# Performance work log

Measured on AMD Instinct MI355X. Metric: run time of the kernel, lower is better.

## Reference

```python
import jax, jax.numpy as jnp
import numpy as np

V, D, L, S = 32000, 512, 4096, 256
LOG2 = float(np.log(2.0))


def _self_conflict(a, span):
    # a: [S, l] bool. Sequential: a[i] = a[i] & ~a[i-1] (using updated values).
    def step1(prev, cur):
        out = cur & ~prev
        return out, out
    first = a[:, 0]
    _, rest = jax.lax.scan(step1, first, a[:, 1:].T)  # scan over token axis
    a = jnp.concatenate([first[:, None], rest.T], axis=1)
    if span == 3:
        # second pass: a[i] = a[i] & ~a[i-2] on the updated array
        def step2(carry, cur):
            pm2, pm1 = carry
            out = cur & ~pm2
            return (pm1, out), out
        _, rest2 = jax.lax.scan(step2, (a[:, 0], a[:, 1]), a[:, 2:].T)
        a = jnp.concatenate([a[:, :2], rest2.T], axis=1)
    return a


def _shift_into(a1, off, L2):
    # hit[j] |= a1[j - off], zeros elsewhere
    B, l1 = a1.shape
    out = jnp.zeros((B, L2), dtype=bool)
    if off >= 0:
        end = min(L2, off + l1)
        return out.at[:, off:end].set(a1[:, :end - off])
    return out.at[:, :l1 + off].set(a1[:, -off:])


def _intersec_conflict(a1, a2, flag=False):
    # a2[j] cleared if any overlapping a1 span is active (set of shifts)
    l1, l2 = a1.shape[1], a2.shape[1]
    hit = jnp.zeros_like(a2)
    for i in range(l2 - l1 + 1):
        hit = hit | _shift_into(a1, i, l2)
    if flag:
        hit = hit | _shift_into(a1, -1, l2) | _shift_into(a1, 2, l2)
    return a2 & ~hit


def _forward(x, embd, w1, b1, w2, b2, w3, b3, g1, g2, g3, align1, align2, align3):
    emb = embd[x]                                   # [1, L, D]
    s2 = (emb[:, 1:] + emb[:, :-1]) / 2             # [1, L-1, D]
    s3 = (emb[:, 2:] + emb[:, 1:-1] + emb[:, :-2]) / 3
    heads = ((emb, w1, b1, g1, align1), (s2, w2, b2, g2, align2), (s3, w3, b3, g3, align3))
    stats, bools = [], []
    for spans, w, b, g, amask in heads:
        logits = spans @ w + b                      # [1, l, 2]
        logp = jax.nn.log_softmax(logits, axis=-1)
        p = jnp.exp(logp)
        nent = -(p * logp).sum(-1) / LOG2           # normalized entropy (2 classes)
        idx = jnp.argmax(logp + g, axis=-1)         # [S, l] Gumbel-max categorical sample
        act = jax.nn.one_hot(idx, 2, dtype=logp.dtype)
        bools.append((idx == 0) & amask[None, :])   # reduce chosen AND aligned
        stats.append((logp, nent, act))

    b1_, b2_, b3_ = bools
    b3_ = _self_conflict(b3_, 3)
    b2_ = _intersec_conflict(b3_, b2_, flag=True)
    b1_ = _intersec_conflict(b3_, b1_)
    b2_ = _self_conflict(b2_, 2)
    b1_ = _intersec_conflict(b2_, b1_)

    logp1, ne1, act1 = stats[0]
    logp2, ne2, _ = stats[1]
    logp3, ne3, _ = stats[2]
    # actions 2/3 are rewritten from the conflict-reduced booleans; action 1 keeps its sample
    act2 = jnp.stack([b2_, ~b2_], axis=-1).astype(logp2.dtype)
    act3 = jnp.stack([b3_, ~b3_], axis=-1).astype(logp3.dtype)

    nll1 = -(act1 * logp1).sum(-1).sum(1)           # [S]
    nll2 = -(act2 * logp2).sum(-1).sum(1)
    nll3 = -(act3 * logp3).sum(-1).sum(1)
    nsamp = act1.shape[0]
    nent = jnp.broadcast_to((ne1.mean(1) + ne2.mean(1) + ne3.mean(1)) / 3.0, (nsamp,))
    return nent, nll1 + nll2 + nll3, b1_, b2_, b3_


def setup_inputs():
    key = jax.random.key(0)
    k = jax.random.split(key, 11)
    x = jax.random.randint(k[0], (1, L), 0, V)
    embd = jax.random.normal(k[1], (V, D), jnp.float32) * 0.02
    w1 = jax.random.normal(k[2], (D, 2), jnp.float32) * 0.05
    w2 = jax.random.normal(k[3], (D, 2), jnp.float32) * 0.05
    w3 = jax.random.normal(k[4], (D, 2), jnp.float32) * 0.05
    b1 = jnp.zeros((2,), jnp.float32)
    b2 = jnp.zeros((2,), jnp.float32)
    b3 = jnp.zeros((2,), jnp.float32)
    g1 = jax.random.gumbel(k[5], (S, L, 2), jnp.float32)
    g2 = jax.random.gumbel(k[6], (S, L - 1, 2), jnp.float32)
    g3 = jax.random.gumbel(k[7], (S, L - 2, 2), jnp.float32)
    align1 = jax.random.randint(k[8], (L,), 0, 2).astype(bool)
    align2 = jax.random.randint(k[9], (L - 1,), 0, 2).astype(bool)
    align3 = jax.random.randint(k[10], (L - 2,), 0, 2).astype(bool)
    return {"x": x, "sample_num": S, "align1": align1, "align2": align2, "align3": align3,
            "embd": embd, "w1": w1, "b1": b1, "w2": w2, "b2": b2, "w3": w3, "b3": b3,
            "g1": g1, "g2": g2, "g3": g3}


def reference(x, sample_num, align1, align2, align3, embd, w1, b1, w2, b2, w3, b3, g1, g2, g3):
    return _forward(x, embd, w1, b1, w2, b2, w3, b3, g1, g2, g3, align1, align2, align3)
```

## Files before the change

### kernel.cpp

```cpp
#include <hip/hip_runtime.h>
#include <stdint.h>

#define L_ 4096
#define S_ 256
#define D_ 512
#define NW 64

static __device__ const float LN2F = 0.69314718055994530942f;

__global__ __launch_bounds__(256)
void k_rows(const int* __restrict__ x, const float* __restrict__ embd,
            const float* __restrict__ w1, const float* __restrict__ b1,
            const float* __restrict__ w2, const float* __restrict__ b2,
            const float* __restrict__ w3, const float* __restrict__ b3,
            float* __restrict__ lp, float* __restrict__ entbuf) {
    const int wid  = threadIdx.x >> 6;
    const int lane = threadIdx.x & 63;
    const int t = blockIdx.x * 4 + wid;
    const int t1 = (t + 1 < L_) ? t + 1 : t;
    const int t2 = (t + 2 < L_) ? t + 2 : t;
    const int d0 = lane * 8;

    const float4* e0p = (const float4*)(embd + (size_t)x[t]  * D_ + d0);
    const float4* e1p = (const float4*)(embd + (size_t)x[t1] * D_ + d0);
    const float4* e2p = (const float4*)(embd + (size_t)x[t2] * D_ + d0);
    float4 e0a = e0p[0], e0b = e0p[1];
    float4 e1a = e1p[0], e1b = e1p[1];
    float4 e2a = e2p[0], e2b = e2p[1];
    const float4* w1p = (const float4*)(w1 + 2 * d0);
    const float4* w2p = (const float4*)(w2 + 2 * d0);
    const float4* w3p = (const float4*)(w3 + 2 * d0);

    float v0[8] = {e0a.x,e0a.y,e0a.z,e0a.w,e0b.x,e0b.y,e0b.z,e0b.w};
    float v1[8] = {e1a.x,e1a.y,e1a.z,e1a.w,e1b.x,e1b.y,e1b.z,e1b.w};
    float v2[8] = {e2a.x,e2a.y,e2a.z,e2a.w,e2b.x,e2b.y,e2b.z,e2b.w};
    float wv1[16], wv2[16], wv3[16];
    for (int q = 0; q < 4; q++) {
        float4 a = w1p[q]; wv1[4*q]=a.x; wv1[4*q+1]=a.y; wv1[4*q+2]=a.z; wv1[4*q+3]=a.w;
        float4 b = w2p[q]; wv2[4*q]=b.x; wv2[4*q+1]=b.y; wv2[4*q+2]=b.z; wv2[4*q+3]=b.w;
        float4 c = w3p[q]; wv3[4*q]=c.x; wv3[4*q+1]=c.y; wv3[4*q+2]=c.z; wv3[4*q+3]=c.w;
    }
    double a0=0,a1=0,a2=0,a3=0,a4=0,a5=0;
    #pragma unroll
    for (int j = 0; j < 8; j++) {
        float s2 = (v1[j] + v0[j]) * 0.5f;
        float s3 = ((v2[j] + v1[j]) + v0[j]) / 3.0f;
        a0 += (double)v0[j] * (double)wv1[2*j];
        a1 += (double)v0[j] * (double)wv1[2*j+1];
        a2 += (double)s2    * (double)wv2[2*j];
        a3 += (double)s2    * (double)wv2[2*j+1];
        a4 += (double)s3    * (double)wv3[2*j];
        a5 += (double)s3    * (double)wv3[2*j+1];
    }
    #pragma unroll
    for (int o = 32; o > 0; o >>= 1) {
        a0 += __shfl_xor(a0, o, 64);
        a1 += __shfl_xor(a1, o, 64);
        a2 += __shfl_xor(a2, o, 64);
        a3 += __shfl_xor(a3, o, 64);
        a4 += __shfl_xor(a4, o, 64);
        a5 += __shfl_xor(a5, o, 64);
    }
    if (lane < 3) {
        double l0, l1; const float* bb;
        if (lane == 0)      { l0 = a0; l1 = a1; bb = b1; }
        else if (lane == 1) { l0 = a2; l1 = a3; bb = b2; }
        else                { l0 = a4; l1 = a5; bb = b3; }
        bool valid = (lane == 0) || (lane == 1 && t < L_-1) || (lane == 2 && t < L_-2);
        float ev = 0.0f;
        if (valid) {
            l0 += (double)bb[0]; l1 += (double)bb[1];
            double m = fmax(l0, l1);
            double sa = l0 - m, sb = l1 - m;
            double lse = log(exp(sa) + exp(sb));
            float p0l = (float)(sa - lse), p1l = (float)(sb - lse);
            lp[2*lane*L_ + t] = p0l; lp[(2*lane+1)*L_ + t] = p1l;
            float p0 = expf(p0l), p1 = expf(p1l);
            ev = -(p0*p0l + p1*p1l) / LN2F;
        }
        entbuf[lane*L_ + t] = ev;
    }
}

__device__ __forceinline__ uint64_t pass1_noc(uint64_t wp) {
    uint64_t o = wp & ~(wp << 1);
    uint64_t h = wp & (wp << 1);
    o |= (o << 2)  & h; h &= (h << 2);
    o |= (o << 4)  & h; h &= (h << 4);
    o |= (o << 8)  & h; h &= (h << 8);
    o |= (o << 16) & h; h &= (h << 16);
    o |= (o << 32) & h;
    return o;
}
__device__ __forceinline__ uint64_t pass2_noc(uint64_t ap) {
    uint64_t o = ap & ~(ap << 2);
    uint64_t h = ap & (ap << 2);
    o |= (o << 4)  & h; h &= (h << 4);
    o |= (o << 8)  & h; h &= (h << 8);
    o |= (o << 16) & h; h &= (h << 16);
    o |= (o << 32) & h;
    return o;
}

__global__ __launch_bounds__(1024)
void k_fused(const float* __restrict__ lp,
             const int* __restrict__ al1, const int* __restrict__ al2, const int* __restrict__ al3,
             const float2* __restrict__ g1, const float2* __restrict__ g2, const float2* __restrict__ g3,
             const float* __restrict__ entbuf, float* __restrict__ out) {
    const int s = blockIdx.x;
    const int tid = threadIdx.x;
    const int lane = tid & 63;
    const int wv = tid >> 6;

    __shared__ uint64_t w1s[NW], w2s[NW], w3s[NW];
    __shared__ uint64_t o1s[NW], o2s[NW], o3s[NW];

    float lp2a[4], lp2b[4], lp3a[4], lp3b[4];
    float nllacc = 0.0f;
    #pragma unroll
    for (int it = 0; it < 4; it++) {
        const int t = it * 1024 + tid;
        float2 v1 = g1[(size_t)s * L_ + t];
        float lp0 = lp[t], lp1v = lp[L_ + t];
        bool raw1 = (lp0 + v1.x) >= (lp1v + v1.y);
        bool m1 = raw1 && (al1[t] != 0);
        nllacc += raw1 ? -lp0 : -lp1v;
        bool m2 = false, m3 = false;
        lp2a[it] = 0.f; lp2b[it] = 0.f; lp3a[it] = 0.f; lp3b[it] = 0.f;
        if (t < L_-1) {
            float2 v2 = g2[(size_t)s * (L_-1) + t];
            float a = lp[2*L_+t], b = lp[3*L_+t];
            lp2a[it] = a; lp2b[it] = b;
            m2 = ((a + v2.x) >= (b + v2.y)) && (al2[t] != 0);
        }
        if (t < L_-2) {
            float2 v3 = g3[(size_t)s * (L_-2) + t];
            float a = lp[4*L_+t], b = lp[5*L_+t];
            lp3a[it] = a; lp3b[it] = b;
            m3 = ((a + v3.x) >= (b + v3.y)) && (al3[t] != 0);
        }
        unsigned long long b1b = __ballot(m1);
        unsigned long long b2b = __ballot(m2);
        unsigned long long b3b = __ballot(m3);
        if (lane == 0) {
            int w = t >> 6;
            w1s[w] = b1b; w2s[w] = b2b; w3s[w] = b3b;
        }
    }
    __syncthreads();

    if (wv == 0) {
        const int j = lane;
        uint64_t w3 = w3s[j];
        uint64_t oA = pass1_noc(w3);
        uint64_t oB = pass1_noc(w3 & ~1ull);
        unsigned F = (unsigned)(oA >> 63) | (((unsigned)(oB >> 63)) << 1);
        #pragma unroll
        for (int d = 1; d < 64; d <<= 1) {
            unsigned P = __shfl_up(F, d, 64);
            if (lane >= d) {
                unsigned la = P & 1, lb = (P >> 1) & 1;
                unsigned ra = F & 1, rb = (F >> 1) & 1;
                F = (la ? rb : ra) | ((lb ? rb : ra) << 1);
            }
        }
        unsigned Fp = __shfl_up(F, 1, 64);
        unsigned cin = (lane == 0) ? 0u : (Fp & 1);
        uint64_t p1 = cin ? oB : oA;

        uint64_t q0 = pass2_noc(p1);
        uint64_t q1 = pass2_noc(p1 & ~1ull);
        uint64_t q2 = pass2_noc(p1 & ~2ull);
        uint64_t q3 = pass2_noc(p1 & ~3ull);
        #define ST_(o) ((unsigned)(((o >> 62) & 1) | (((o >> 63) & 1) << 1)))
        unsigned G = ST_(q0) | (ST_(q1) << 2) | (ST_(q2) << 4) | (ST_(q3) << 6);
        #undef ST_
        #pragma unroll
        for (int d = 1; d < 64; d <<= 1) {
            unsigned P = __shfl_up(G, d, 64);
            if (lane >= d) {
                unsigned H = 0;
                #pragma unroll
                for (int xx = 0; xx < 4; xx++) {
                    unsigned m = (P >> (2 * xx)) & 3;
                    H |= ((G >> (2 * m)) & 3) << (2 * xx);
                }
                G = H;
            }
        }
        unsigned Gp = __shfl_up(G, 1, 64);
        unsigned s2in = (lane == 0) ? 0u : (Gp & 3);
        uint64_t B3 = (s2in == 0) ? q0 : (s2in == 1) ? q1 : (s2in == 2) ? q2 : q3;

        uint64_t B3m1 = __shfl_up((unsigned long long)B3, 1, 64); if (lane == 0)  B3m1 = 0;
        uint64_t B3nx = __shfl_down((unsigned long long)B3, 1, 64); if (lane == 63) B3nx = 0;
        uint64_t sh1 = (B3 << 1) | (B3m1 >> 63);
        uint64_t sh2 = (B3 << 2) | (B3m1 >> 62);
        uint64_t shm = (B3 >> 1) | (B3nx << 63);
        uint64_t hit2 = B3 | sh1 | sh2 | shm;

        uint64_t in2 = w2s[j] & ~hit2;
        uint64_t oA2 = pass1_noc(in2);
        uint64_t oB2 = pass1_noc(in2 & ~1ull);
        unsigned F2 = (unsigned)(oA2 >> 63) | (((unsigned)(oB2 >> 63)) << 1);
        #pragma unroll
        for (int d = 1; d < 64; d <<= 1) {
            unsigned P = __shfl_up(F2, d, 64);
            if (lane >= d) {
                unsigned la = P & 1, lb = (P >> 1) & 1;
                unsigned ra = F2 & 1, rb = (F2 >> 1) & 1;
                F2 = (la ? rb : ra) | ((lb ? rb : ra) << 1);
            }
        }
        unsigned F2p = __shfl_up(F2, 1, 64);
        unsigned cin2 = (lane == 0) ? 0u : (F2p & 1);
        uint64_t B2 = cin2 ? oB2 : oA2;

        uint64_t B2m1 = __shfl_up((unsigned long long)B2, 1, 64); if (lane == 0) B2m1 = 0;
        uint64_t hit1 = B3 | sh1 | sh2 | B2 | ((B2 << 1) | (B2m1 >> 63));
        uint64_t B1 = w1s[j] & ~hit1;

        o1s[j] = B1; o2s[j] = B2; o3s[j] = B3;
    }
    __syncthreads();

    float* b1o = out + 2*S_;
    float* b2o = b1o + (size_t)S_ * L_;
    float* b3o = b2o + (size_t)S_ * (L_-1);
    #pragma unroll
    for (int it = 0; it < 4; it++) {
        const int t = it * 1024 + tid;
        const int w = t >> 6, b = t & 63;
        b1o[(size_t)s*L_ + t] = (float)((o1s[w] >> b) & 1);
        if (t < L_-1) {
            unsigned bit = (unsigned)((o2s[w] >> b) & 1);
            b2o[(size_t)s*(L_-1) + t] = (float)bit;
            nllacc += bit ? -lp2a[it] : -lp2b[it];
        }
        if (t < L_-2) {
            unsigned bit = (unsigned)((o3s[w] >> b) & 1);
            b3o[(size_t)s*(L_-2) + t] = (float)bit;
            nllacc += bit ? -lp3a[it] : -lp3b[it];
        }
    }
    #pragma unroll
    for (int o = 32; o > 0; o >>= 1) nllacc += __shfl_xor(nllacc, o, 64);
    __shared__ float red[16];
    if (lane == 0) red[wv] = nllacc;
    __syncthreads();
    if (tid == 0) {
        float tot = 0.f;
        #pragma unroll
        for (int i = 0; i < 16; i++) tot += red[i];
        out[S_ + s] = tot;
    }

    if (s == 0 && wv == 0) {
        double s1 = 0, s2d = 0, s3d = 0;
        for (int t = lane; t < L_; t += 64) {
            s1  += (double)entbuf[t];
            s2d += (double)entbuf[L_ + t];
            s3d += (double)entbuf[2*L_ + t];
        }
        #pragma unroll
        for (int o = 32; o > 0; o >>= 1) {
            s1  += __shfl_xor(s1, o, 64);
            s2d += __shfl_xor(s2d, o, 64);
            s3d += __shfl_xor(s3d, o, 64);
        }
        float v = (float)((s1 / (double)L_ + s2d / (double)(L_-1) + s3d / (double)(L_-2)) / 3.0);
        #pragma unroll
        for (int i = 0; i < 4; i++) out[lane + 64*i] = v;
    }
}

extern "C" void kernel_launch(void* const* d_in, const int* in_sizes, int n_in,
                              void* d_out, int out_size, void* d_ws, size_t ws_size,
                              hipStream_t stream) {
    const int*   x    = (const int*)d_in[0];
    const int*   al1  = (const int*)d_in[2];
    const int*   al2  = (const int*)d_in[3];
    const int*   al3  = (const int*)d_in[4];
    const float* embd = (const float*)d_in[5];
    const float* w1   = (const float*)d_in[6];
    const float* b1   = (const float*)d_in[7];
    const float* w2   = (const float*)d_in[8];
    const float* b2   = (const float*)d_in[9];
    const float* w3   = (const float*)d_in[10];
    const float* b3   = (const float*)d_in[11];
    const float2* g1  = (const float2*)d_in[12];
    const float2* g2  = (const float2*)d_in[13];
    const float2* g3  = (const float2*)d_in[14];
    float* out = (float*)d_out;

    float* lp     = (float*)d_ws;
    float* entbuf = lp + 6 * L_;

    hipLaunchKernelGGL(k_rows, dim3(1024), dim3(256), 0, stream,
                       x, embd, w1, b1, w2, b2, w3, b3, lp, entbuf);
    hipLaunchKernelGGL(k_fused, dim3(S_), dim3(1024), 0, stream,
                       lp, al1, al2, al3, g1, g2, g3, entbuf, out);
}
```

Before: 168.4 us.

## Fuse row logit kernel and sampling kernel into one cooperative launch with grid sync

Merges the per-token logit and entropy kernel into the per-sample kernel through a cooperative launch. Each of the 256 blocks first computes 16 tokens' logits, then a grid-wide sync separates that phase from the sampling phase. The log-prob buffer is also changed to interleaved float2 pairs so each head's pair comes from one load. This removes one kernel launch and the gap between launches, at the cost of a grid barrier and of requiring all 256 blocks of 1024 threads to be co-resident.

```diff
diff --git a/kernel.cpp b/kernel.cpp
--- a/kernel.cpp
+++ b/kernel.cpp
@@ -1,5 +1,8 @@
 #include <hip/hip_runtime.h>
+#include <hip/hip_cooperative_groups.h>
 #include <stdint.h>
+
+namespace cg = cooperative_groups;
 
 #define L_ 4096
 #define S_ 256
@@ -7,80 +10,6 @@
 #define NW 64
 
 static __device__ const float LN2F = 0.69314718055994530942f;
-
-__global__ __launch_bounds__(256)
-void k_rows(const int* __restrict__ x, const float* __restrict__ embd,
-            const float* __restrict__ w1, const float* __restrict__ b1,
-            const float* __restrict__ w2, const float* __restrict__ b2,
-            const float* __restrict__ w3, const float* __restrict__ b3,
-            float* __restrict__ lp, float* __restrict__ entbuf) {
-    const int wid  = threadIdx.x >> 6;
-    const int lane = threadIdx.x & 63;
-    const int t = blockIdx.x * 4 + wid;
-    const int t1 = (t + 1 < L_) ? t + 1 : t;
-    const int t2 = (t + 2 < L_) ? t + 2 : t;
-    const int d0 = lane * 8;
-
-    const float4* e0p = (const float4*)(embd + (size_t)x[t]  * D_ + d0);
-    const float4* e1p = (const float4*)(embd + (size_t)x[t1] * D_ + d0);
-    const float4* e2p = (const float4*)(embd + (size_t)x[t2] * D_ + d0);
-    float4 e0a = e0p[0], e0b = e0p[1];
-    float4 e1a = e1p[0], e1b = e1p[1];
-    float4 e2a = e2p[0], e2b = e2p[1];
-    const float4* w1p = (const float4*)(w1 + 2 * d0);
-    const float4* w2p = (const float4*)(w2 + 2 * d0);
-    const float4* w3p = (const float4*)(w3 + 2 * d0);
-
-    float v0[8] = {e0a.x,e0a.y,e0a.z,e0a.w,e0b.x,e0b.y,e0b.z,e0b.w};
-    float v1[8] = {e1a.x,e1a.y,e1a.z,e1a.w,e1b.x,e1b.y,e1b.z,e1b.w};
-    float v2[8] = {e2a.x,e2a.y,e2a.z,e2a.w,e2b.x,e2b.y,e2b.z,e2b.w};
-    float wv1[16], wv2[16], wv3[16];
-    for (int q = 0; q < 4; q++) {
-        float4 a = w1p[q]; wv1[4*q]=a.x; wv1[4*q+1]=a.y; wv1[4*q+2]=a.z; wv1[4*q+3]=a.w;
-        float4 b = w2p[q]; wv2[4*q]=b.x; wv2[4*q+1]=b.y; wv2[4*q+2]=b.z; wv2[4*q+3]=b.w;
-        float4 c = w3p[q]; wv3[4*q]=c.x; wv3[4*q+1]=c.y; wv3[4*q+2]=c.z; wv3[4*q+3]=c.w;
-    }
-    double a0=0,a1=0,a2=0,a3=0,a4=0,a5=0;
-    #pragma unroll
-    for (int j = 0; j < 8; j++) {
-        float s2 = (v1[j] + v0[j]) * 0.5f;
-        float s3 = ((v2[j] + v1[j]) + v0[j]) / 3.0f;
-        a0 += (double)v0[j] * (double)wv1[2*j];
-        a1 += (double)v0[j] * (double)wv1[2*j+1];
-        a2 += (double)s2    * (double)wv2[2*j];
-        a3 += (double)s2    * (double)wv2[2*j+1];
-        a4 += (double)s3    * (double)wv3[2*j];
-        a5 += (double)s3    * (double)wv3[2*j+1];
-    }
-    #pragma unroll
-    for (int o = 32; o > 0; o >>= 1) {
-        a0 += __shfl_xor(a0, o, 64);
-        a1 += __shfl_xor(a1, o, 64);
-        a2 += __shfl_xor(a2, o, 64);
-        a3 += __shfl_xor(a3, o, 64);
-        a4 += __shfl_xor(a4, o, 64);
-        a5 += __shfl_xor(a5, o, 64);
-    }
-    if (lane < 3) {
-        double l0, l1; const float* bb;
-        if (lane == 0)      { l0 = a0; l1 = a1; bb = b1; }
-        else if (lane == 1) { l0 = a2; l1 = a3; bb = b2; }
-        else                { l0 = a4; l1 = a5; bb = b3; }
-        bool valid = (lane == 0) || (lane == 1 && t < L_-1) || (lane == 2 && t < L_-2);
-        float ev = 0.0f;
-        if (valid) {
-            l0 += (double)bb[0]; l1 += (double)bb[1];
-            double m = fmax(l0, l1);
-            double sa = l0 - m, sb = l1 - m;
-            double lse = log(exp(sa) + exp(sb));
-            float p0l = (float)(sa - lse), p1l = (float)(sb - lse);
-            lp[2*lane*L_ + t] = p0l; lp[(2*lane+1)*L_ + t] = p1l;
-            float p0 = expf(p0l), p1 = expf(p1l);
-            ev = -(p0*p0l + p1*p1l) / LN2F;
-        }
-        entbuf[lane*L_ + t] = ev;
-    }
-}
 
 __device__ __forceinline__ uint64_t pass1_noc(uint64_t wp) {
     uint64_t o = wp & ~(wp << 1);
@@ -103,41 +32,114 @@
 }
 
 __global__ __launch_bounds__(1024)
-void k_fused(const float* __restrict__ lp,
-             const int* __restrict__ al1, const int* __restrict__ al2, const int* __restrict__ al3,
-             const float2* __restrict__ g1, const float2* __restrict__ g2, const float2* __restrict__ g3,
-             const float* __restrict__ entbuf, float* __restrict__ out) {
+void k_all(const int* __restrict__ x, const float* __restrict__ embd,
+           const float* __restrict__ w1, const float* __restrict__ b1,
+           const float* __restrict__ w2, const float* __restrict__ b2,
+           const float* __restrict__ w3, const float* __restrict__ b3,
+           const int* __restrict__ al1, const int* __restrict__ al2, const int* __restrict__ al3,
+           const float2* __restrict__ g1, const float2* __restrict__ g2, const float2* __restrict__ g3,
+           float2* __restrict__ lph, float* __restrict__ entbuf, float* __restrict__ out) {
+    const int tid  = threadIdx.x;
+    const int lane = tid & 63;
+    const int wv   = tid >> 6;
+
+    {
+        const int t = blockIdx.x * 16 + wv;
+        const int t1 = (t + 1 < L_) ? t + 1 : t;
+        const int t2 = (t + 2 < L_) ? t + 2 : t;
+        const int d0 = lane * 8;
+
+        const float4* e0p = (const float4*)(embd + (size_t)x[t]  * D_ + d0);
+        const float4* e1p = (const float4*)(embd + (size_t)x[t1] * D_ + d0);
+        const float4* e2p = (const float4*)(embd + (size_t)x[t2] * D_ + d0);
+        float4 e0a = e0p[0], e0b = e0p[1];
+        float4 e1a = e1p[0], e1b = e1p[1];
+        float4 e2a = e2p[0], e2b = e2p[1];
+        const float4* w1p = (const float4*)(w1 + 2 * d0);
+        const float4* w2p = (const float4*)(w2 + 2 * d0);
+        const float4* w3p = (const float4*)(w3 + 2 * d0);
+
+        float v0[8] = {e0a.x,e0a.y,e0a.z,e0a.w,e0b.x,e0b.y,e0b.z,e0b.w};
+        float v1[8] = {e1a.x,e1a.y,e1a.z,e1a.w,e1b.x,e1b.y,e1b.z,e1b.w};
+        float v2[8] = {e2a.x,e2a.y,e2a.z,e2a.w,e2b.x,e2b.y,e2b.z,e2b.w};
+        float wv1[16], wv2[16], wv3[16];
+        for (int q = 0; q < 4; q++) {
+            float4 a = w1p[q]; wv1[4*q]=a.x; wv1[4*q+1]=a.y; wv1[4*q+2]=a.z; wv1[4*q+3]=a.w;
+            float4 b = w2p[q]; wv2[4*q]=b.x; wv2[4*q+1]=b.y; wv2[4*q+2]=b.z; wv2[4*q+3]=b.w;
+            float4 c = w3p[q]; wv3[4*q]=c.x; wv3[4*q+1]=c.y; wv3[4*q+2]=c.z; wv3[4*q+3]=c.w;
+        }
+        double a0=0,a1=0,a2=0,a3=0,a4=0,a5=0;
+        #pragma unroll
+        for (int j = 0; j < 8; j++) {
+            float s2 = (v1[j] + v0[j]) * 0.5f;
+            float s3 = ((v2[j] + v1[j]) + v0[j]) / 3.0f;
+            a0 += (double)v0[j] * (double)wv1[2*j];
+            a1 += (double)v0[j] * (double)wv1[2*j+1];
+            a2 += (double)s2    * (double)wv2[2*j];
+            a3 += (double)s2    * (double)wv2[2*j+1];
+            a4 += (double)s3    * (double)wv3[2*j];
+            a5 += (double)s3    * (double)wv3[2*j+1];
+        }
+        #pragma unroll
+        for (int o = 32; o > 0; o >>= 1) {
+            a0 += __shfl_xor(a0, o, 64);
+            a1 += __shfl_xor(a1, o, 64);
+            a2 += __shfl_xor(a2, o, 64);
+            a3 += __shfl_xor(a3, o, 64);
+            a4 += __shfl_xor(a4, o, 64);
+            a5 += __shfl_xor(a5, o, 64);
+        }
+        if (lane < 3) {
+            double l0, l1; const float* bb;
+            if (lane == 0)      { l0 = a0; l1 = a1; bb = b1; }
+            else if (lane == 1) { l0 = a2; l1 = a3; bb = b2; }
+            else                { l0 = a4; l1 = a5; bb = b3; }
+            bool valid = (lane == 0) || (lane == 1 && t < L_-1) || (lane == 2 && t < L_-2);
+            float ev = 0.0f;
+            if (valid) {
+                l0 += (double)bb[0]; l1 += (double)bb[1];
+                double m = fmax(l0, l1);
+                double sa = l0 - m, sb = l1 - m;
+                double lse = log(exp(sa) + exp(sb));
+                float p0l = (float)(sa - lse), p1l = (float)(sb - lse);
+                lph[lane*L_ + t] = make_float2(p0l, p1l);
+                float p0 = expf(p0l), p1 = expf(p1l);
+                ev = -(p0*p0l + p1*p1l) / LN2F;
+            }
+            entbuf[lane*L_ + t] = ev;
+        }
+    }
+
+    cg::this_grid().sync();
+
     const int s = blockIdx.x;
-    const int tid = threadIdx.x;
-    const int lane = tid & 63;
-    const int wv = tid >> 6;
-
     __shared__ uint64_t w1s[NW], w2s[NW], w3s[NW];
     __shared__ uint64_t o1s[NW], o2s[NW], o3s[NW];
 
-    float lp2a[4], lp2b[4], lp3a[4], lp3b[4];
+    float2 lph2v[4], lph3v[4];
     float nllacc = 0.0f;
     #pragma unroll
     for (int it = 0; it < 4; it++) {
         const int t = it * 1024 + tid;
         float2 v1 = g1[(size_t)s * L_ + t];
-        float lp0 = lp[t], lp1v = lp[L_ + t];
-        bool raw1 = (lp0 + v1.x) >= (lp1v + v1.y);
+        float2 p1v = lph[t];
+        bool raw1 = (p1v.x + v1.x) >= (p1v.y + v1.y);
         bool m1 = raw1 && (al1[t] != 0);
-        nllacc += raw1 ? -lp0 : -lp1v;
+        nllacc += raw1 ? -p1v.x : -p1v.y;
         bool m2 = false, m3 = false;
-        lp2a[it] = 0.f; lp2b[it] = 0.f; lp3a[it] = 0.f; lp3b[it] = 0.f;
+        lph2v[it] = make_float2(0.f, 0.f);
+        lph3v[it] = make_float2(0.f, 0.f);
         if (t < L_-1) {
             float2 v2 = g2[(size_t)s * (L_-1) + t];
-            float a = lp[2*L_+t], b = lp[3*L_+t];
-            lp2a[it] = a; lp2b[it] = b;
-            m2 = ((a + v2.x) >= (b + v2.y)) && (al2[t] != 0);
+            float2 p2v = lph[L_ + t];
+            lph2v[it] = p2v;
+            m2 = ((p2v.x + v2.x) >= (p2v.y + v2.y)) && (al2[t] != 0);
         }
         if (t < L_-2) {
             float2 v3 = g3[(size_t)s * (L_-2) + t];
-            float a = lp[4*L_+t], b = lp[5*L_+t];
-            lp3a[it] = a; lp3b[it] = b;
-            m3 = ((a + v3.x) >= (b + v3.y)) && (al3[t] != 0);
+            float2 p3v = lph[2*L_ + t];
+            lph3v[it] = p3v;
+            m3 = ((p3v.x + v3.x) >= (p3v.y + v3.y)) && (al3[t] != 0);
         }
         unsigned long long b1b = __ballot(m1);
         unsigned long long b2b = __ballot(m2);
@@ -151,9 +153,9 @@
 
     if (wv == 0) {
         const int j = lane;
-        uint64_t w3 = w3s[j];
-        uint64_t oA = pass1_noc(w3);
-        uint64_t oB = pass1_noc(w3 & ~1ull);
+        uint64_t w3w = w3s[j];
+        uint64_t oA = pass1_noc(w3w);
+        uint64_t oB = pass1_noc(w3w & ~1ull);
         unsigned F = (unsigned)(oA >> 63) | (((unsigned)(oB >> 63)) << 1);
         #pragma unroll
         for (int d = 1; d < 64; d <<= 1) {
@@ -235,12 +237,12 @@
         if (t < L_-1) {
             unsigned bit = (unsigned)((o2s[w] >> b) & 1);
             b2o[(size_t)s*(L_-1) + t] = (float)bit;
-            nllacc += bit ? -lp2a[it] : -lp2b[it];
+            nllacc += bit ? -lph2v[it].x : -lph2v[it].y;
         }
         if (t < L_-2) {
             unsigned bit = (unsigned)((o3s[w] >> b) & 1);
             b3o[(size_t)s*(L_-2) + t] = (float)bit;
-            nllacc += bit ? -lp3a[it] : -lp3b[it];
+            nllacc += bit ? -lph3v[it].x : -lph3v[it].y;
         }
     }
     #pragma unroll
@@ -293,11 +295,15 @@
     const float2* g3  = (const float2*)d_in[14];
     float* out = (float*)d_out;
 
-    float* lp     = (float*)d_ws;
-    float* entbuf = lp + 6 * L_;
-
-    hipLaunchKernelGGL(k_rows, dim3(1024), dim3(256), 0, stream,
-                       x, embd, w1, b1, w2, b2, w3, b3, lp, entbuf);
-    hipLaunchKernelGGL(k_fused, dim3(S_), dim3(1024), 0, stream,
-                       lp, al1, al2, al3, g1, g2, g3, entbuf, out);
+    float2* lph   = (float2*)d_ws;
+    float* entbuf = (float*)(lph + 3 * L_);
+
+    void* args[] = {
+        (void*)&x, (void*)&embd,
+        (void*)&w1, (void*)&b1, (void*)&w2, (void*)&b2, (void*)&w3, (void*)&b3,
+        (void*)&al1, (void*)&al2, (void*)&al3,
+        (void*)&g1, (void*)&g2, (void*)&g3,
+        (void*)&lph, (void*)&entbuf, (void*)&out
+    };
+    hipLaunchCooperativeKernel((const void*)k_all, dim3(S_), dim3(1024), args, 0, stream);
 }
```

Measured after the change: 222.5 us. 32.1% more time.
